# Optimization experiments

Hardware: AMD Instinct MI355X
Metric: run time of the kernel (lower is better)

Reference implementation:

```python
import jax, jax.numpy as jnp
import numpy as np

A, M, Q, H, T = 4096, 64, 64, 64, 4
BOX_L = 20.0


def _pairwise_displacements(positions, box):
    # Minimal-image pairwise displacements. dr[i, j] = r_j - r_i (PBC-wrapped).
    diff = positions[None, :, :] - positions[:, None, :]          # [A, A, 3]
    frac = diff @ jnp.linalg.inv(box)                             # fractional coords
    frac = frac - jnp.round(frac)                                 # minimal image
    dr = frac @ box                                               # [A, A, 3]
    rij = jnp.linalg.norm(dr, axis=-1)                            # [A, A]
    return dr, rij


def _per_type_mlp(descriptors, Z, W0, b0, atom_mask):
    # a_i = q_i @ W0[Z_i] + b0[Z_i]; h = tanh(a) * mask
    W0_t = W0[Z]                                                  # [A, Q, H]
    b0_t = b0[Z]                                                  # [A, H]
    h = jnp.tanh(jnp.einsum('nd,ndh->nh', descriptors, W0_t) + b0_t)
    return h * atom_mask[:, None], W0_t


def _calc_forces(h, gradients, W1_t, W0_t, neighbor_mask):
    # dU_i/dR_j via chain rule through tanh MLP.
    dtanh = 1.0 - jnp.square(h)                                   # [A, H]
    de_da = dtanh * W1_t                                          # [A, H]
    de_dq = jnp.einsum('nh,nqh->nq', de_da, W0_t)                 # [A, Q]
    forces = jnp.einsum('nq,nmcq->nmc', de_dq, gradients)         # [A, M, 3]
    return forces * neighbor_mask[:, :, None]


def setup_inputs() -> dict:
    key = jax.random.key(0)
    ks = jax.random.split(key, 12)
    descriptors = jax.random.normal(ks[0], (A, Q), jnp.float32)
    gradients = jax.random.normal(ks[1], (A, M, 3, Q), jnp.float32)
    grad_index = jax.random.randint(ks[2], (A, M), 0, A, jnp.int32)
    positions = jax.random.uniform(ks[3], (A, 3), jnp.float32) * BOX_L
    Z = jax.random.randint(ks[4], (A,), 0, T, jnp.int32)
    box = jnp.eye(3, dtype=jnp.float32) * BOX_L
    atom_mask = jnp.ones((A,), jnp.float32)
    neighbor_mask = jnp.ones((A, M), jnp.float32)
    s = 0.05
    return {
        'descriptors': descriptors, 'gradients': gradients,
        'grad_index': grad_index, 'positions': positions, 'Z': Z,
        'box': box, 'atom_mask': atom_mask, 'neighbor_mask': neighbor_mask,
        'W0': jax.random.normal(ks[5], (T, Q, H), jnp.float32) * s,
        'b0': jnp.zeros((T, H), jnp.float32),
        'W1': jax.random.normal(ks[6], (T, H), jnp.float32) * s,
        'b1': jnp.zeros((), jnp.float32),
        'W0_pol': jax.random.normal(ks[7], (T, Q, H), jnp.float32) * s,
        'b0_pol': jnp.zeros((T, H), jnp.float32),
        'W1_pol': jax.random.normal(ks[8], (T, H), jnp.float32) * s,
        'b1_pol': jnp.zeros((), jnp.float32),
    }


def reference(descriptors, gradients, grad_index, positions, Z, box,
              atom_mask, neighbor_mask, W0, b0, W1, b1,
              W0_pol, b0_pol, W1_pol, b1_pol):
    # Tensor ANN
    h, W0_t = _per_type_mlp(descriptors, Z, W0, b0, atom_mask)
    W1_t = W1[Z]                                                  # [A, H]
    forces = _calc_forces(h, gradients, W1_t, W0_t, neighbor_mask)  # [A, M, 3]

    # Pairwise displacements + neighbor gather (tf.gather_nd equivalent)
    dr, _rij = _pairwise_displacements(positions, box)            # [A, A, 3]
    rows = jnp.arange(A)[:, None]                                 # [A, 1]
    dr_gathered = dr[rows, grad_index]                            # [A, M, 3]

    # Scalar (pol) ANN -> isotropic diagonal contribution
    h_pol, _ = _per_type_mlp(descriptors, Z, W0_pol, b0_pol, atom_mask)
    F_pol = (jnp.sum(h_pol * W1_pol[Z], axis=1) + b1_pol) * atom_mask
    scalar_sum = jnp.sum(F_pol)

    # Anisotropic virial: -sum_{n,m} dr (x) forces
    pol_outer = -jnp.einsum('nma,nmb->nmab', dr_gathered, forces)
    pol_outer = pol_outer * neighbor_mask[:, :, None, None]
    pm = jnp.sum(pol_outer, axis=(0, 1))                          # [3, 3]

    pol = jnp.stack([pm[0, 0], pm[1, 1], pm[2, 2], pm[0, 1], pm[1, 2], pm[2, 0]])
    pol = pol + jnp.stack([scalar_sum, scalar_sum, scalar_sum,
                           jnp.zeros((), pol.dtype), jnp.zeros((), pol.dtype),
                           jnp.zeros((), pol.dtype)])
    return pol
```

## Files before the change

kernel.cpp:

```cpp
#include <hip/hip_runtime.h>
#include <hip/hip_bf16.h>
#include <math.h>

#define NA 4096
#define NM 64
#define NQ 64
#define NH 64

#define WS_FLOATS (10 * NA)

__global__ __launch_bounds__(256) void tnep_main(
    const float* __restrict__ desc,
    const float* __restrict__ grad,
    const int*   __restrict__ gidx,
    const float* __restrict__ pos,
    const int*   __restrict__ Zp,
    const float* __restrict__ box,
    const float* __restrict__ amaskp,
    const float* __restrict__ nmaskp,
    const float* __restrict__ W0,
    const float* __restrict__ b0,
    const float* __restrict__ W1,
    const float* __restrict__ W0p,
    const float* __restrict__ b0p,
    const float* __restrict__ W1p,
    const float* __restrict__ b1p,
    float* __restrict__ ws)
{
    const int n    = blockIdx.x;
    const int tid  = threadIdx.x;
    const int w    = tid >> 6;
    const int lane = tid & 63;
    const int z    = Zp[n];

    __shared__ float sW0[NQ * 65];
    __shared__ float sdesc[NQ];
    __shared__ float sde_da[NH];
    __shared__ float sde_dq[NQ];
    __shared__ float swdr[NM * 4];
    __shared__ float sacc[4][12];

    const float4* W0v = reinterpret_cast<const float4*>(W0 + (size_t)z * NQ * NH);
#pragma unroll
    for (int i = 0; i < 4; ++i) {
        int f = i * 256 + tid;
        float4 v = W0v[f];
        int q  = f >> 4;
        int h0 = (f & 15) * 4;
        float* p = &sW0[q * 65 + h0];
        p[0] = v.x; p[1] = v.y; p[2] = v.z; p[3] = v.w;
    }
    if (w == 0) sdesc[lane] = desc[n * NQ + lane];
    if (w == 1) {
        int g = gidx[n * NM + lane];
        float Lx = box[0], Ly = box[4], Lz = box[8];
        float dx = pos[g * 3 + 0] - pos[n * 3 + 0];
        float dy = pos[g * 3 + 1] - pos[n * 3 + 1];
        float dz = pos[g * 3 + 2] - pos[n * 3 + 2];
        dx -= Lx * rintf(dx * (1.0f / Lx));
        dy -= Ly * rintf(dy * (1.0f / Ly));
        dz -= Lz * rintf(dz * (1.0f / Lz));
        float nm = nmaskp[n * NM + lane];
        float wt = -nm * nm;
        swdr[lane * 4 + 0] = wt * dx;
        swdr[lane * 4 + 1] = wt * dy;
        swdr[lane * 4 + 2] = wt * dz;
        swdr[lane * 4 + 3] = 0.0f;
    }
    __syncthreads();

    if (w == 0) {
        float amask = amaskp[n];
        float a_t = b0[z * NH + lane];
#pragma unroll 8
        for (int q = 0; q < NQ; ++q)
            a_t = fmaf(sdesc[q], sW0[q * 65 + lane], a_t);
        float hT = tanhf(a_t) * amask;
        sde_da[lane] = (1.0f - hT * hT) * W1[z * NH + lane];
    } else if (w == 2) {
        float amask = amaskp[n];
        float a_p = b0p[z * NH + lane];
        const float* W0prow = W0p + (size_t)z * NQ * NH;
        const float* drow   = desc + (size_t)n * NQ;
#pragma unroll 8
        for (int q = 0; q < NQ; ++q)
            a_p = fmaf(drow[q], W0prow[q * NH + lane], a_p);
        float hP = tanhf(a_p) * amask;
        float fp = hP * W1p[z * NH + lane];
#pragma unroll
        for (int s = 1; s < 64; s <<= 1) fp += __shfl_xor(fp, s, 64);
        if (lane == 0) ws[9 * NA + n] = (fp + b1p[0]) * amask;
    }
    __syncthreads();

    if (w == 0) {
        float dq = 0.0f;
#pragma unroll 8
        for (int h = 0; h < NH; ++h)
            dq = fmaf(sde_da[h], sW0[lane * 65 + h], dq);
        sde_dq[lane] = dq;
    }
    __syncthreads();

    const int msub = lane >> 4;
    const int q4   = lane & 15;
    float4 dq4 = *reinterpret_cast<const float4*>(&sde_dq[4 * q4]);
    float acc[3][3] = {{0.f,0.f,0.f},{0.f,0.f,0.f},{0.f,0.f,0.f}};

    const int m0 = w * 16;
    const float4* gbase = reinterpret_cast<const float4*>(grad)
                          + ((size_t)n * NM + m0) * 48 + msub * 48 + q4;
#pragma unroll
    for (int gset = 0; gset < 4; ++gset) {
        const float4* gp = gbase + gset * 192;
        const int m = m0 + gset * 4 + msub;
        float wd0 = swdr[m * 4 + 0];
        float wd1 = swdr[m * 4 + 1];
        float wd2 = swdr[m * 4 + 2];
#pragma unroll
        for (int c = 0; c < 3; ++c) {
            float4 g4 = gp[c * 16];
            float s = fmaf(dq4.x, g4.x, fmaf(dq4.y, g4.y,
                      fmaf(dq4.z, g4.z, dq4.w * g4.w)));
            acc[0][c] = fmaf(s, wd0, acc[0][c]);
            acc[1][c] = fmaf(s, wd1, acc[1][c]);
            acc[2][c] = fmaf(s, wd2, acc[2][c]);
        }
    }

#pragma unroll
    for (int a = 0; a < 3; ++a)
#pragma unroll
        for (int c = 0; c < 3; ++c) {
            float v = acc[a][c];
#pragma unroll
            for (int s = 1; s < 64; s <<= 1) v += __shfl_xor(v, s, 64);
            if (lane == 0) sacc[w][a * 3 + c] = v;
        }
    __syncthreads();
    if (tid < 9)
        ws[tid * NA + n] = sacc[0][tid] + sacc[1][tid] + sacc[2][tid] + sacc[3][tid];
}

__global__ __launch_bounds__(640) void tnep_reduce(const float* __restrict__ ws,
                                                   float* __restrict__ out)
{
    __shared__ float sred[10];
    const int w    = threadIdx.x >> 6;
    const int lane = threadIdx.x & 63;

    const float4* p = reinterpret_cast<const float4*>(ws + (size_t)w * NA);
    float s = 0.f;
#pragma unroll
    for (int i = 0; i < 16; ++i) {
        float4 v = p[lane + 64 * i];
        s += (v.x + v.y) + (v.z + v.w);
    }
#pragma unroll
    for (int t = 1; t < 64; t <<= 1) s += __shfl_xor(s, t, 64);
    if (lane == 0) sred[w] = s;
    __syncthreads();
    if (threadIdx.x == 0) {
        float S = sred[9];
        out[0] = sred[0] + S;
        out[1] = sred[4] + S;
        out[2] = sred[8] + S;
        out[3] = sred[1];
        out[4] = sred[5];
        out[5] = sred[6];
    }
}

__global__ __launch_bounds__(64) void tnep_mono(
    const float* __restrict__ desc,
    const float* __restrict__ grad,
    const int*   __restrict__ gidx,
    const float* __restrict__ pos,
    const int*   __restrict__ Zp,
    const float* __restrict__ box,
    const float* __restrict__ amaskp,
    const float* __restrict__ nmaskp,
    const float* __restrict__ W0,
    const float* __restrict__ b0,
    const float* __restrict__ W1,
    const float* __restrict__ W0p,
    const float* __restrict__ b0p,
    const float* __restrict__ W1p,
    const float* __restrict__ b1p,
    float* __restrict__ out)
{
    const int n    = blockIdx.x;
    const int lane = threadIdx.x;
    const int z    = Zp[n];
    const float amask = amaskp[n];

    __shared__ float sdesc[NQ];
    __shared__ float sW0[NQ * 65];
    __shared__ float sde_da[NH];
    __shared__ float sde_dq[NQ];
    __shared__ float sdr[NM * 4];

    sdesc[lane] = desc[n * NQ + lane];
    const float4* W0v = reinterpret_cast<const float4*>(W0 + (size_t)z * NQ * NH);
#pragma unroll
    for (int i = 0; i < 16; ++i) {
        float4 v = W0v[i * 64 + lane];
        int q  = 4 * i + (lane >> 4);
        int h0 = 4 * (lane & 15);
        float* p = &sW0[q * 65 + h0];
        p[0] = v.x; p[1] = v.y; p[2] = v.z; p[3] = v.w;
    }
    {
        int g = gidx[n * NM + lane];
        float Lx = box[0], Ly = box[4], Lz = box[8];
        float dx = pos[g * 3 + 0] - pos[n * 3 + 0];
        float dy = pos[g * 3 + 1] - pos[n * 3 + 1];
        float dz = pos[g * 3 + 2] - pos[n * 3 + 2];
        dx -= Lx * rintf(dx * (1.0f / Lx));
        dy -= Ly * rintf(dy * (1.0f / Ly));
        dz -= Lz * rintf(dz * (1.0f / Lz));
        float nm = nmaskp[n * NM + lane];
        float wt = -nm * nm;
        sdr[lane * 4 + 0] = wt * dx;
        sdr[lane * 4 + 1] = wt * dy;
        sdr[lane * 4 + 2] = wt * dz;
        sdr[lane * 4 + 3] = 0.0f;
    }
    __syncthreads();

    float a_t = b0 [z * NH + lane];
    float a_p = b0p[z * NH + lane];
    const float* W0prow = W0p + (size_t)z * NQ * NH;
#pragma unroll 8
    for (int q = 0; q < NQ; ++q) {
        float d = sdesc[q];
        a_t = fmaf(d, sW0[q * 65 + lane], a_t);
        a_p = fmaf(d, W0prow[q * NH + lane], a_p);
    }
    float hT = tanhf(a_t) * amask;
    float hP = tanhf(a_p) * amask;
    sde_da[lane] = (1.0f - hT * hT) * W1[z * NH + lane];
    float fp = hP * W1p[z * NH + lane];
#pragma unroll
    for (int s = 1; s < 64; s <<= 1) fp += __shfl_xor(fp, s, 64);
    __syncthreads();

    float dq = 0.0f;
#pragma unroll 8
    for (int h = 0; h < NH; ++h)
        dq = fmaf(sde_da[h], sW0[lane * 65 + h], dq);
    sde_dq[lane] = dq;
    __syncthreads();

    const int msub = lane >> 4;
    const int q4   = lane & 15;
    float4 dq4 = *reinterpret_cast<const float4*>(&sde_dq[4 * q4]);
    float acc[3][3] = {{0.f,0.f,0.f},{0.f,0.f,0.f},{0.f,0.f,0.f}};
    const float4* gbase = reinterpret_cast<const float4*>(grad)
                          + (size_t)n * NM * 48 + msub * 48 + q4;
#pragma unroll
    for (int gset = 0; gset < 16; ++gset) {
        const float4* gp = gbase + gset * 192;
        const int m = gset * 4 + msub;
        float wd0 = sdr[m * 4 + 0];
        float wd1 = sdr[m * 4 + 1];
        float wd2 = sdr[m * 4 + 2];
#pragma unroll
        for (int c = 0; c < 3; ++c) {
            float4 g4 = gp[c * 16];
            float s = fmaf(dq4.x, g4.x, fmaf(dq4.y, g4.y, fmaf(dq4.z, g4.z, dq4.w * g4.w)));
            acc[0][c] = fmaf(s, wd0, acc[0][c]);
            acc[1][c] = fmaf(s, wd1, acc[1][c]);
            acc[2][c] = fmaf(s, wd2, acc[2][c]);
        }
    }
    float fpv = (fp + b1p[0]) * amask;
#pragma unroll
    for (int a = 0; a < 3; ++a)
#pragma unroll
        for (int c = 0; c < 3; ++c) {
            float v = acc[a][c];
#pragma unroll
            for (int s = 1; s < 64; s <<= 1) v += __shfl_xor(v, s, 64);
            acc[a][c] = v;
        }
    if (lane == 0) {
        atomicAdd(out + 0, acc[0][0] + fpv);
        atomicAdd(out + 1, acc[1][1] + fpv);
        atomicAdd(out + 2, acc[2][2] + fpv);
        atomicAdd(out + 3, acc[0][1]);
        atomicAdd(out + 4, acc[1][2]);
        atomicAdd(out + 5, acc[2][0]);
    }
}

__global__ void tnep_zero(float* out)
{
    if (threadIdx.x < 6) out[threadIdx.x] = 0.f;
}

extern "C" void kernel_launch(void* const* d_in, const int* in_sizes, int n_in,
                              void* d_out, int out_size, void* d_ws, size_t ws_size,
                              hipStream_t stream)
{
    const float* desc  = (const float*)d_in[0];
    const float* grad  = (const float*)d_in[1];
    const int*   gidx  = (const int*)  d_in[2];
    const float* pos   = (const float*)d_in[3];
    const int*   Zp    = (const int*)  d_in[4];
    const float* box   = (const float*)d_in[5];
    const float* amask = (const float*)d_in[6];
    const float* nmask = (const float*)d_in[7];
    const float* W0    = (const float*)d_in[8];
    const float* b0    = (const float*)d_in[9];
    const float* W1    = (const float*)d_in[10];
    const float* W0p   = (const float*)d_in[12];
    const float* b0p   = (const float*)d_in[13];
    const float* W1p   = (const float*)d_in[14];
    const float* b1p   = (const float*)d_in[15];
    float* out = (float*)d_out;
    float* ws  = (float*)d_ws;

    if (ws_size >= (size_t)WS_FLOATS * sizeof(float)) {
        tnep_main<<<NA, 256, 0, stream>>>(desc, grad, gidx, pos, Zp, box, amask, nmask,
                                          W0, b0, W1, W0p, b0p, W1p, b1p, ws);
        tnep_reduce<<<1, 640, 0, stream>>>(ws, out);
    } else {
        tnep_zero<<<1, 64, 0, stream>>>(out);
        tnep_mono<<<NA, 64, 0, stream>>>(desc, grad, gidx, pos, Zp, box, amask, nmask,
                                         W0, b0, W1, W0p, b0p, W1p, b1p, out);
    }
}
```

Measured before the change: 47.38 us.

## Split fused kernel into per-atom prep kernel and gradient streaming kernel

```diff
diff --git a/kernel.cpp b/kernel.cpp
--- a/kernel.cpp
+++ b/kernel.cpp
@@ -7,11 +7,10 @@
 #define NQ 64
 #define NH 64
 
-#define WS_FLOATS (10 * NA)
-
-__global__ __launch_bounds__(256) void tnep_main(
+#define WS_FLOATS (330 * NA)
+
+__global__ __launch_bounds__(256) void tnep_prep(
     const float* __restrict__ desc,
-    const float* __restrict__ grad,
     const int*   __restrict__ gidx,
     const float* __restrict__ pos,
     const int*   __restrict__ Zp,
@@ -33,12 +32,13 @@
     const int lane = tid & 63;
     const int z    = Zp[n];
 
+    float* PARTT = ws;
+    float* DQ    = ws + 10 * NA;
+    float* WDR   = ws + 74 * NA;
+
     __shared__ float sW0[NQ * 65];
     __shared__ float sdesc[NQ];
     __shared__ float sde_da[NH];
-    __shared__ float sde_dq[NQ];
-    __shared__ float swdr[NM * 4];
-    __shared__ float sacc[4][12];
 
     const float4* W0v = reinterpret_cast<const float4*>(W0 + (size_t)z * NQ * NH);
 #pragma unroll
@@ -62,10 +62,8 @@
         dz -= Lz * rintf(dz * (1.0f / Lz));
         float nm = nmaskp[n * NM + lane];
         float wt = -nm * nm;
-        swdr[lane * 4 + 0] = wt * dx;
-        swdr[lane * 4 + 1] = wt * dy;
-        swdr[lane * 4 + 2] = wt * dz;
-        swdr[lane * 4 + 3] = 0.0f;
+        float4 wd = make_float4(wt * dx, wt * dy, wt * dz, 0.0f);
+        *reinterpret_cast<float4*>(WDR + (size_t)n * 256 + lane * 4) = wd;
     }
     __syncthreads();
 
@@ -89,7 +87,7 @@
         float fp = hP * W1p[z * NH + lane];
 #pragma unroll
         for (int s = 1; s < 64; s <<= 1) fp += __shfl_xor(fp, s, 64);
-        if (lane == 0) ws[9 * NA + n] = (fp + b1p[0]) * amask;
+        if (lane == 0) PARTT[9 * NA + n] = (fp + b1p[0]) * amask;
     }
     __syncthreads();
 
@@ -98,13 +96,32 @@
 #pragma unroll 8
         for (int h = 0; h < NH; ++h)
             dq = fmaf(sde_da[h], sW0[lane * 65 + h], dq);
-        sde_dq[lane] = dq;
-    }
+        DQ[(size_t)n * 64 + lane] = dq;
+    }
+}
+
+__global__ __launch_bounds__(256, 8) void tnep_stream(
+    const float* __restrict__ grad,
+    float* __restrict__ ws)
+{
+    const int n    = blockIdx.x;
+    const int tid  = threadIdx.x;
+    const int w    = tid >> 6;
+    const int lane = tid & 63;
+
+    float* PARTT = ws;
+    const float* DQ  = ws + 10 * NA;
+    const float* WDR = ws + 74 * NA;
+
+    __shared__ float swdr[NM * 4];
+    __shared__ float sacc[4][12];
+
+    swdr[tid] = WDR[(size_t)n * 256 + tid];
+    float4 dq4 = *reinterpret_cast<const float4*>(DQ + (size_t)n * 64 + 4 * (lane & 15));
     __syncthreads();
 
     const int msub = lane >> 4;
     const int q4   = lane & 15;
-    float4 dq4 = *reinterpret_cast<const float4*>(&sde_dq[4 * q4]);
     float acc[3][3] = {{0.f,0.f,0.f},{0.f,0.f,0.f},{0.f,0.f,0.f}};
 
     const int m0 = w * 16;
@@ -114,17 +131,15 @@
     for (int gset = 0; gset < 4; ++gset) {
         const float4* gp = gbase + gset * 192;
         const int m = m0 + gset * 4 + msub;
-        float wd0 = swdr[m * 4 + 0];
-        float wd1 = swdr[m * 4 + 1];
-        float wd2 = swdr[m * 4 + 2];
+        float4 wd = *reinterpret_cast<const float4*>(&swdr[m * 4]);
 #pragma unroll
         for (int c = 0; c < 3; ++c) {
             float4 g4 = gp[c * 16];
             float s = fmaf(dq4.x, g4.x, fmaf(dq4.y, g4.y,
                       fmaf(dq4.z, g4.z, dq4.w * g4.w)));
-            acc[0][c] = fmaf(s, wd0, acc[0][c]);
-            acc[1][c] = fmaf(s, wd1, acc[1][c]);
-            acc[2][c] = fmaf(s, wd2, acc[2][c]);
+            acc[0][c] = fmaf(s, wd.x, acc[0][c]);
+            acc[1][c] = fmaf(s, wd.y, acc[1][c]);
+            acc[2][c] = fmaf(s, wd.z, acc[2][c]);
         }
     }
 
@@ -139,7 +154,7 @@
         }
     __syncthreads();
     if (tid < 9)
-        ws[tid * NA + n] = sacc[0][tid] + sacc[1][tid] + sacc[2][tid] + sacc[3][tid];
+        PARTT[tid * NA + n] = sacc[0][tid] + sacc[1][tid] + sacc[2][tid] + sacc[3][tid];
 }
 
 __global__ __launch_bounds__(640) void tnep_reduce(const float* __restrict__ ws,
@@ -322,8 +337,9 @@
     float* ws  = (float*)d_ws;
 
     if (ws_size >= (size_t)WS_FLOATS * sizeof(float)) {
-        tnep_main<<<NA, 256, 0, stream>>>(desc, grad, gidx, pos, Zp, box, amask, nmask,
+        tnep_prep<<<NA, 256, 0, stream>>>(desc, gidx, pos, Zp, box, amask, nmask,
                                           W0, b0, W1, W0p, b0p, W1p, b1p, ws);
+        tnep_stream<<<NA, 256, 0, stream>>>(grad, ws);
         tnep_reduce<<<1, 640, 0, stream>>>(ws, out);
     } else {
         tnep_zero<<<1, 64, 0, stream>>>(out);
```

New measurement: 51.77 us. 9.3% more time.
